# Optimization experiments

Hardware: AMD Instinct MI355X
Metric: run time of the kernel (lower is better)

## Reference

```python
import jax, jax.numpy as jnp
import numpy as np

B, N, DIM, H, DH = 2, 2048, 1024, 16, 64
SOFTCAP = 50.0
SCALE = DH ** -0.5
EPS = 1e-12


def _rmsnorm(x, gamma):
    # F.normalize (l2norm over last dim) * sqrt(dim) * (gamma + 1)
    norm = jnp.maximum(jnp.linalg.norm(x, axis=-1, keepdims=True), EPS)
    return (x / norm) * (DIM ** 0.5) * (gamma + 1.0)


def _rotate_half(t):
    # interleaved pairs: (x1, x2) -> (-x2, x1), as in rotary_embedding_torch
    t = t.reshape(*t.shape[:-1], -1, 2)
    x1, x2 = t[..., 0], t[..., 1]
    return jnp.stack((-x2, x1), axis=-1).reshape(*t.shape[:-2], -1)


def _apply_rotary(freqs, t):
    # freqs: [n, d] broadcast over [b, h, n, d]
    return t * jnp.cos(freqs) + _rotate_half(t) * jnp.sin(freqs)


def setup_inputs() -> dict:
    key = jax.random.key(0)
    k0, k1, k2, k3, k4 = jax.random.split(key, 5)
    x = jax.random.normal(k0, (B, N, DIM), jnp.float32)
    gamma = jax.random.normal(k1, (DIM,), jnp.float32) * 0.02
    w_qkv = jax.random.normal(k2, (DIM, 3 * H * DH), jnp.float32) * 0.02
    w_out = jax.random.normal(k3, (H * DH, DIM), jnp.float32) * 0.02
    rotary_emb = jax.random.normal(k4, (N, DH), jnp.float32)
    attn_mask = jnp.broadcast_to(jnp.tril(jnp.ones((N, N), bool)), (B, N, N))
    return {"x": x, "attn_mask": attn_mask, "rotary_emb": rotary_emb,
            "gamma": gamma, "w_qkv": w_qkv, "w_out": w_out}


def reference(x, attn_mask, rotary_emb, gamma, w_qkv, w_out):
    x = _rmsnorm(x, gamma)
    qkv = (x @ w_qkv).reshape(B, N, 3, H, DH)        # b n (qkv h d)
    qkv = jnp.transpose(qkv, (2, 0, 3, 1, 4))        # qkv b h n d
    q, k, v = qkv[0], qkv[1], qkv[2]
    q = _apply_rotary(rotary_emb, q)
    k = _apply_rotary(rotary_emb, k)
    q = q * SCALE
    sim = jnp.einsum('bhid,bhjd->bhij', q, k)
    sim = jnp.tanh(sim / SOFTCAP) * SOFTCAP          # softclamp
    mask_value = -jnp.finfo(sim.dtype).max
    sim = jnp.where(attn_mask[:, None, :, :], sim, mask_value)
    attn = jax.nn.softmax(sim, axis=-1)
    out = jnp.einsum('bhij,bhjd->bhid', attn, v)
    out = jnp.transpose(out, (0, 2, 1, 3)).reshape(B, N, H * DH)  # b n (h d)
    return out @ w_out
```

## Files before the change

### kernel.cpp

```cpp
#include <hip/hip_runtime.h>
#include <hip/hip_bf16.h>

typedef unsigned short u16;
typedef unsigned int u32;
typedef __bf16 bf16x8 __attribute__((ext_vector_type(8)));
typedef float f32x4 __attribute__((ext_vector_type(4)));

#define NB 2
#define NSEQ 2048
#define NDIM 1024
#define NH 16
#define NDH 64

static __device__ __forceinline__ u16 f2bf(float f) {
  return __builtin_bit_cast(u16, (__bf16)f);
}
static __device__ __forceinline__ float bf2f(u16 u) {
  union { u32 u; float f; } a; a.u = ((u32)u) << 16; return a.f;
}
static __device__ __forceinline__ bf16x8 ldbf8(const u16* p) {
  return *(const bf16x8*)p;
}
static __device__ __forceinline__ f32x4 mfma16(bf16x8 a, bf16x8 b, f32x4 c) {
  return __builtin_amdgcn_mfma_f32_16x16x32_bf16(a, b, c, 0, 0, 0);
}
static __device__ __forceinline__ float fexp2(float x) {
  return __builtin_amdgcn_exp2f(x);
}
#define GLDS(g, d) __builtin_amdgcn_global_load_lds(                         \
    (const __attribute__((address_space(1))) void*)(g),                      \
    (__attribute__((address_space(3))) void*)(d), 16, 0, 0)

__global__ __launch_bounds__(256) void k_transpose(const float* __restrict__ in,
                                                   u16* __restrict__ out,
                                                   int R, int C) {
  __shared__ u16 tile[64][65];
  const int r0 = blockIdx.x * 64, c0 = blockIdx.y * 64;
  const int t = threadIdx.x;
  const int tr = t >> 6;
  const int tc = t & 63;
#pragma unroll 4
  for (int p = 0; p < 16; p++) {
    int r = p * 4 + tr;
    tile[r][tc] = f2bf(in[(size_t)(r0 + r) * C + (c0 + tc)]);
  }
  __syncthreads();
#pragma unroll 4
  for (int p = 0; p < 16; p++) {
    int rr = p * 4 + tr;
    out[(size_t)(c0 + rr) * R + (r0 + tc)] = tile[tc][rr];
  }
}

__global__ __launch_bounds__(256) void k_rmsnorm(const float* __restrict__ x,
                                                 const float* __restrict__ gamma,
                                                 u16* __restrict__ xn) {
  __shared__ float part[4];
  const int row = blockIdx.x;
  const int t = threadIdx.x;
  const float4 v = ((const float4*)(x + (size_t)row * NDIM))[t];
  float ss = v.x * v.x + v.y * v.y + v.z * v.z + v.w * v.w;
#pragma unroll
  for (int off = 1; off < 64; off <<= 1) ss += __shfl_xor(ss, off, 64);
  if ((t & 63) == 0) part[t >> 6] = ss;
  __syncthreads();
  const float tot = part[0] + part[1] + part[2] + part[3];
  const float scale = 32.0f / fmaxf(sqrtf(tot), 1e-12f);
  const float4 g = ((const float4*)gamma)[t];
  u16 o0 = f2bf(v.x * scale * (g.x + 1.0f));
  u16 o1 = f2bf(v.y * scale * (g.y + 1.0f));
  u16 o2 = f2bf(v.z * scale * (g.z + 1.0f));
  u16 o3 = f2bf(v.w * scale * (g.w + 1.0f));
  uint2 pv;
  pv.x = (u32)o0 | ((u32)o1 << 16);
  pv.y = (u32)o2 | ((u32)o3 << 16);
  *(uint2*)(xn + (size_t)row * NDIM + t * 4) = pv;
}

template <int EPI>
__global__ __launch_bounds__(256) void k_gemm_bt(const u16* __restrict__ A,
                                                 const u16* __restrict__ BT,
                                                 float* __restrict__ Of,
                                                 u16* __restrict__ O0,
                                                 u16* __restrict__ O1,
                                                 u16* __restrict__ O2) {
  constexpr int KD = 1024, BK = 64, NT = KD / BK;
  __shared__ u16 As[128 * BK];
  __shared__ u16 Bs[128 * BK];
  const int m0 = blockIdx.x * 128, n0 = blockIdx.y * 128;
  const int t = threadIdx.x;
  const int w = t >> 6, l = t & 63, lo = l & 15, hi = l >> 4;
  const int wr = (w >> 1) * 64, wc = (w & 1) * 64;
  const int srow = w * 32 + (l >> 3);
  const int sch  = (l & 7) ^ (l >> 3);
  const u16* ag = A  + (size_t)(m0 + srow) * KD + sch * 8;
  const u16* bg = BT + (size_t)(n0 + srow) * KD + sch * 8;
  u16* asd = As + w * 2048;
  u16* bsd = Bs + w * 2048;
  f32x4 acc[4][4] = {};
  for (int kt = 0; kt < NT; kt++) {
    const int k0 = kt * BK;
    __syncthreads();
#pragma unroll
    for (int i = 0; i < 4; i++) {
      GLDS(ag + k0 + i * 8 * KD, asd + i * 512);
      GLDS(bg + k0 + i * 8 * KD, bsd + i * 512);
    }
    __syncthreads();
    bf16x8 af[4][2], bb[4][2];
#pragma unroll
    for (int i = 0; i < 4; i++) {
      const int Ra = wr + i * 16 + lo, xa = Ra & 7;
      af[i][0] = ldbf8(&As[Ra * 64 + ((hi ^ xa) << 3)]);
      af[i][1] = ldbf8(&As[Ra * 64 + (((4 + hi) ^ xa) << 3)]);
      const int Rb = wc + i * 16 + lo, xb = Rb & 7;
      bb[i][0] = ldbf8(&Bs[Rb * 64 + ((hi ^ xb) << 3)]);
      bb[i][1] = ldbf8(&Bs[Rb * 64 + (((4 + hi) ^ xb) << 3)]);
    }
#pragma unroll
    for (int i = 0; i < 4; i++)
#pragma unroll
      for (int j = 0; j < 4; j++) {
        acc[i][j] = mfma16(af[i][0], bb[j][0], acc[i][j]);
        acc[i][j] = mfma16(af[i][1], bb[j][1], acc[i][j]);
      }
  }
#pragma unroll
  for (int i = 0; i < 4; i++) {
#pragma unroll
    for (int j = 0; j < 4; j++) {
      const int gr0 = m0 + wr + i * 16 + hi * 4;
      const int gc = n0 + wc + j * 16 + lo;
#pragma unroll
      for (int r = 0; r < 4; r++) {
        const int row = gr0 + r;
        if (EPI == 0) {
          Of[(size_t)row * 1024 + gc] = acc[i][j][r];
        } else {
          const u16 bv = f2bf(acc[i][j][r]);
          const int which = gc >> 10, rem = gc & 1023;
          const int h = rem >> 6, dh = rem & 63;
          const int b = row >> 11, ns = row & 2047;
          if (which == 2) {
            O2[(((size_t)b * NH + h) * NDH + dh) * NSEQ + ns] = bv;
          } else {
            const size_t idx = ((((size_t)b * NH + h) * NSEQ) + ns) * NDH + dh;
            (which == 0 ? O0 : O1)[idx] = bv;
          }
        }
      }
    }
  }
}

__global__ __launch_bounds__(256) void k_rotprep(const float* __restrict__ rot,
                                                 float4* __restrict__ tab) {
  const int i = blockIdx.x * 256 + threadIdx.x;
  const int n = i >> 5, p = i & 31;
  const float fe = rot[n * NDH + 2 * p], fo = rot[n * NDH + 2 * p + 1];
  float ce, se, co, so;
  __sincosf(fe, &se, &ce);
  __sincosf(fo, &so, &co);
  tab[i] = make_float4(ce, se, co, so);
}

__global__ __launch_bounds__(256) void k_rotary(u16* __restrict__ qb,
                                                u16* __restrict__ kb,
                                                const float4* __restrict__ tab) {
  const int gi = blockIdx.x * 256 + threadIdx.x;
  const int half = gi >> 19;
  const int i = gi & ((1 << 19) - 1);
  u16* buf = half ? kb : qb;
  const float scale = half ? 1.0f : 0.125f;
  const int p0 = (i & 7) * 4;
  const int n = (i >> 3) & (NSEQ - 1);
  union { uint4 v; u16 s[8]; } u;
  u.v = *(const uint4*)(buf + (size_t)i * 8);
  union { uint4 v; u16 s[8]; } o;
#pragma unroll
  for (int pp = 0; pp < 4; pp++) {
    const float4 tb = tab[n * 32 + p0 + pp];
    const float a = bf2f(u.s[2 * pp]), b = bf2f(u.s[2 * pp + 1]);
    o.s[2 * pp]     = f2bf((a * tb.x - b * tb.y) * scale);
    o.s[2 * pp + 1] = f2bf((b * tb.z + a * tb.w) * scale);
  }
  *(uint4*)(buf + (size_t)i * 8) = o.v;
}

#define KCH(row, ch) ((((ch) ^ ((row) & 7)) * 8))
__global__ __launch_bounds__(128) void k_attn(const u16* __restrict__ Q,
                                              const u16* __restrict__ K,
                                              const u16* __restrict__ Vt,
                                              u16* __restrict__ O) {
  __shared__ u16 Ks[2][2048];
  __shared__ u16 Vs[2][2048];
  __shared__ u16 Ps[2][16][40];
  const int qt = 63 - (blockIdx.x >> 5);
  const int bh = blockIdx.x & 31;
  const int b = bh >> 4, h = bh & 15;
  const size_t base = (size_t)bh * (NSEQ * NDH);
  const int t = threadIdx.x;
  const int w = t >> 6, l = t & 63, lq = l & 15, hf = l >> 4;
  const int rl = l >> 3;
  const int sc8 = ((l & 7) ^ rl) * 8;
  const int vr = l >> 2;
  const int q0 = qt * 32;
  const int nkt = qt + 1;
  const int rowg = q0 + w * 16 + hf * 4;

  bf16x8 aq0, aq1;
  {
    const u16* qp = Q + base + (size_t)(q0 + w * 16 + lq) * NDH;
    aq0 = ldbf8(qp + hf * 8);
    aq1 = ldbf8(qp + 32 + hf * 8);
  }
  f32x4 accO[4] = {};
  float lp[4] = {0.f, 0.f, 0.f, 0.f};

#define STAGE(bb, kt_)                                                        \
  {                                                                           \
    _Pragma("unroll")                                                         \
    for (int i_ = 0; i_ < 2; i_++) {                                          \
      const int ii = w * 2 + i_;                                              \
      GLDS(K + base + (size_t)((kt_) * 32 + ii * 8 + rl) * NDH + sc8,         \
           &Ks[bb][ii * 512]);                                                \
      const int dR = ii * 16 + vr;                                            \
      const int vc = (((l & 3) ^ (dR & 3) ^ ((dR >> 2) & 3))) * 8;            \
      GLDS(Vt + base + (size_t)dR * NSEQ + (kt_) * 32 + vc,                   \
           &Vs[bb][ii * 512]);                                                \
    }                                                                         \
  }

  int cur = 0;
  STAGE(0, 0);

  for (int kt = 0; kt < nkt; kt++) {
    __syncthreads();
    if (kt + 1 < nkt) STAGE(cur ^ 1, kt + 1);
    const u16* ks = Ks[cur];
    const u16* vs = Vs[cur];

    f32x4 s[2];
#pragma unroll
    for (int nt = 0; nt < 2; nt++) {
      const int kr = nt * 16 + lq;
      f32x4 z = {};
      z = mfma16(aq0, ldbf8(&ks[kr * 64 + KCH(kr, hf)]), z);
      z = mfma16(aq1, ldbf8(&ks[kr * 64 + KCH(kr, 4 + hf)]), z);
      s[nt] = z;
    }
    const bool diag = (kt == qt);
#pragma unroll
    for (int nt = 0; nt < 2; nt++) {
      const int col = kt * 32 + nt * 16 + lq;
#pragma unroll
      for (int r = 0; r < 4; r++) {
        const float v = s[nt][r];
        const float uu = v * v;
        const float poly = fmaf(uu, fmaf(uu, 2.1333333e-8f, -1.3333333e-4f), 1.0f);
        float p = fexp2(v * 1.44269504f * poly);
        if (diag && col > rowg + r) p = 0.0f;
        s[nt][r] = p;
        lp[r] += p;
      }
    }
#pragma unroll
    for (int nt = 0; nt < 2; nt++)
#pragma unroll
      for (int r = 0; r < 4; r++)
        Ps[w][hf * 4 + r][nt * 16 + lq] = f2bf(s[nt][r]);

    const bf16x8 ap0 = ldbf8(&Ps[w][lq][hf * 8]);
    const int vph = (hf ^ (lq & 3) ^ ((lq >> 2) & 3)) * 8;
#pragma unroll
    for (int dt = 0; dt < 4; dt++) {
      const int d = dt * 16 + lq;
      accO[dt] = mfma16(ap0, ldbf8(&vs[d * 32 + vph]), accO[dt]);
    }
    cur ^= 1;
  }
  float lr[4];
#pragma unroll
  for (int r = 0; r < 4; r++) {
    float lv = lp[r];
    lv += __shfl_xor(lv, 1, 64);
    lv += __shfl_xor(lv, 2, 64);
    lv += __shfl_xor(lv, 4, 64);
    lv += __shfl_xor(lv, 8, 64);
    lr[r] = __builtin_amdgcn_rcpf(lv);
  }
#pragma unroll
  for (int dt = 0; dt < 4; dt++) {
#pragma unroll
    for (int r = 0; r < 4; r++) {
      const int row = rowg + r;
      const float v = accO[dt][r] * lr[r];
      const size_t idx = (((size_t)(b * NSEQ + row)) * NH + h) * NDH + dt * 16 + lq;
      O[idx] = f2bf(v);
    }
  }
#undef STAGE
}

extern "C" void kernel_launch(void* const* d_in, const int* in_sizes, int n_in,
                              void* d_out, int out_size, void* d_ws, size_t ws_size,
                              hipStream_t stream) {
  const float* x     = (const float*)d_in[0];
  const float* rot   = (const float*)d_in[2];
  const float* gamma = (const float*)d_in[3];
  const float* wqkv  = (const float*)d_in[4];
  const float* wout  = (const float*)d_in[5];

  char* ws = (char*)d_ws;
  u16* xn    = (u16*)(ws);
  u16* wqkvT = (u16*)(ws + (size_t)( 8u << 20));
  u16* woutT = (u16*)(ws + (size_t)(14u << 20));
  u16* qb    = (u16*)(ws + (size_t)(16u << 20));
  u16* kb    = (u16*)(ws + (size_t)(24u << 20));
  u16* vt    = (u16*)(ws + (size_t)(32u << 20));
  float4* rtab = (float4*)(ws);
  u16* ob    = xn;

  k_transpose<<<dim3(16, 48), 256, 0, stream>>>(wqkv, wqkvT, 1024, 3072);
  k_transpose<<<dim3(16, 16), 256, 0, stream>>>(wout, woutT, 1024, 1024);
  k_rmsnorm<<<4096, 256, 0, stream>>>(x, gamma, xn);
  k_gemm_bt<1><<<dim3(32, 24), 256, 0, stream>>>(xn, wqkvT, nullptr, qb, kb, vt);
  k_rotprep<<<256, 256, 0, stream>>>(rot, rtab);
  k_rotary<<<4096, 256, 0, stream>>>(qb, kb, rtab);
  k_attn<<<2048, 128, 0, stream>>>(qb, kb, vt, ob);
  k_gemm_bt<0><<<dim3(32, 8), 256, 0, stream>>>(ob, woutT, (float*)d_out, nullptr, nullptr, nullptr);
}
```

Before: 143.4 us.

## Pair causal query tiles per block, widen KV tiles, fuse Q rotary into attention

```diff
diff --git a/kernel.cpp b/kernel.cpp
--- a/kernel.cpp
+++ b/kernel.cpp
@@ -164,139 +164,175 @@
   tab[i] = make_float4(ce, se, co, so);
 }
 
-__global__ __launch_bounds__(256) void k_rotary(u16* __restrict__ qb,
-                                                u16* __restrict__ kb,
+__global__ __launch_bounds__(256) void k_rotary(u16* __restrict__ kb,
                                                 const float4* __restrict__ tab) {
-  const int gi = blockIdx.x * 256 + threadIdx.x;
-  const int half = gi >> 19;
-  const int i = gi & ((1 << 19) - 1);
-  u16* buf = half ? kb : qb;
-  const float scale = half ? 1.0f : 0.125f;
+  const int i = blockIdx.x * 256 + threadIdx.x;
   const int p0 = (i & 7) * 4;
   const int n = (i >> 3) & (NSEQ - 1);
   union { uint4 v; u16 s[8]; } u;
-  u.v = *(const uint4*)(buf + (size_t)i * 8);
+  u.v = *(const uint4*)(kb + (size_t)i * 8);
   union { uint4 v; u16 s[8]; } o;
 #pragma unroll
   for (int pp = 0; pp < 4; pp++) {
     const float4 tb = tab[n * 32 + p0 + pp];
     const float a = bf2f(u.s[2 * pp]), b = bf2f(u.s[2 * pp + 1]);
-    o.s[2 * pp]     = f2bf((a * tb.x - b * tb.y) * scale);
-    o.s[2 * pp + 1] = f2bf((b * tb.z + a * tb.w) * scale);
-  }
-  *(uint4*)(buf + (size_t)i * 8) = o.v;
+    o.s[2 * pp]     = f2bf(a * tb.x - b * tb.y);
+    o.s[2 * pp + 1] = f2bf(b * tb.z + a * tb.w);
+  }
+  *(uint4*)(kb + (size_t)i * 8) = o.v;
 }
 
 #define KCH(row, ch) ((((ch) ^ ((row) & 7)) * 8))
 __global__ __launch_bounds__(128) void k_attn(const u16* __restrict__ Q,
                                               const u16* __restrict__ K,
                                               const u16* __restrict__ Vt,
+                                              const float4* __restrict__ rtab,
                                               u16* __restrict__ O) {
-  __shared__ u16 Ks[2][2048];
-  __shared__ u16 Vs[2][2048];
-  __shared__ u16 Ps[2][16][40];
-  const int qt = 63 - (blockIdx.x >> 5);
+  __shared__ u16 Ks[2][4096];
+  __shared__ u16 Vs[2][4096];
+  __shared__ u16 Ps[2][16][64];
+  const int pr = blockIdx.x >> 5;
   const int bh = blockIdx.x & 31;
   const int b = bh >> 4, h = bh & 15;
   const size_t base = (size_t)bh * (NSEQ * NDH);
   const int t = threadIdx.x;
   const int w = t >> 6, l = t & 63, lq = l & 15, hf = l >> 4;
+
   const int rl = l >> 3;
   const int sc8 = ((l & 7) ^ rl) * 8;
-  const int vr = l >> 2;
-  const int q0 = qt * 32;
-  const int nkt = qt + 1;
-  const int rowg = q0 + w * 16 + hf * 4;
-
-  bf16x8 aq0, aq1;
-  {
-    const u16* qp = Q + base + (size_t)(q0 + w * 16 + lq) * NDH;
-    aq0 = ldbf8(qp + hf * 8);
-    aq1 = ldbf8(qp + 32 + hf * 8);
-  }
-  f32x4 accO[4] = {};
-  float lp[4] = {0.f, 0.f, 0.f, 0.f};
+
+  const u16* kR[4];
+  const u16* vR[4];
+#pragma unroll
+  for (int i_ = 0; i_ < 4; i_++) {
+    const int R_ = (w * 4 + i_) * 8 + rl;
+    kR[i_] = K + base + (size_t)R_ * NDH + sc8;
+    vR[i_] = Vt + base + (size_t)R_ * NSEQ + sc8;
+  }
 
 #define STAGE(bb, kt_)                                                        \
   {                                                                           \
     _Pragma("unroll")                                                         \
-    for (int i_ = 0; i_ < 2; i_++) {                                          \
-      const int ii = w * 2 + i_;                                              \
-      GLDS(K + base + (size_t)((kt_) * 32 + ii * 8 + rl) * NDH + sc8,         \
-           &Ks[bb][ii * 512]);                                                \
-      const int dR = ii * 16 + vr;                                            \
-      const int vc = (((l & 3) ^ (dR & 3) ^ ((dR >> 2) & 3))) * 8;            \
-      GLDS(Vt + base + (size_t)dR * NSEQ + (kt_) * 32 + vc,                   \
-           &Vs[bb][ii * 512]);                                                \
+    for (int i_ = 0; i_ < 4; i_++) {                                          \
+      GLDS(kR[i_] + (size_t)(kt_) * (64 * NDH), &Ks[bb][(w * 4 + i_) * 512]); \
+      GLDS(vR[i_] + (kt_) * 64, &Vs[bb][(w * 4 + i_) * 512]);                 \
     }                                                                         \
   }
 
   int cur = 0;
-  STAGE(0, 0);
-
-  for (int kt = 0; kt < nkt; kt++) {
+  STAGE(0, pr * 0);
+
+#pragma unroll
+  for (int half = 0; half < 2; half++) {
+    const int qt = half ? (63 - pr) : pr;
+    const int q0 = qt * 32;
+    const int nkt = (qt >> 1) + 1;
+    const int ktd = nkt - 1;
+    const int rowg = q0 + w * 16 + hf * 4;
+
+    bf16x8 aq0, aq1;
+    {
+      const u16* qp = Q + base + (size_t)(q0 + w * 16 + lq) * NDH;
+      union { bf16x8 v; u16 s[8]; } r0, r1, o0, o1;
+      r0.v = ldbf8(qp + hf * 8);
+      r1.v = ldbf8(qp + 32 + hf * 8);
+      const float4* rt = rtab + (size_t)(q0 + w * 16 + lq) * 32;
+#pragma unroll
+      for (int m = 0; m < 4; m++) {
+        const float4 t0 = rt[hf * 4 + m];
+        const float a0 = bf2f(r0.s[2 * m]), b0 = bf2f(r0.s[2 * m + 1]);
+        o0.s[2 * m]     = f2bf((a0 * t0.x - b0 * t0.y) * 0.125f);
+        o0.s[2 * m + 1] = f2bf((b0 * t0.z + a0 * t0.w) * 0.125f);
+        const float4 t1 = rt[16 + hf * 4 + m];
+        const float a1 = bf2f(r1.s[2 * m]), b1 = bf2f(r1.s[2 * m + 1]);
+        o1.s[2 * m]     = f2bf((a1 * t1.x - b1 * t1.y) * 0.125f);
+        o1.s[2 * m + 1] = f2bf((b1 * t1.z + a1 * t1.w) * 0.125f);
+      }
+      aq0 = o0.v;
+      aq1 = o1.v;
+    }
+    f32x4 accO[4] = {};
+    float lp[4] = {0.f, 0.f, 0.f, 0.f};
+
+#define QTILE(KT, DIAG)                                                       \
+    {                                                                         \
+      const u16* ks = Ks[cur];                                                \
+      const u16* vs = Vs[cur];                                                \
+      f32x4 s[4];                                                             \
+      _Pragma("unroll")                                                       \
+      for (int nt = 0; nt < 4; nt++) {                                        \
+        const int kr = nt * 16 + lq;                                          \
+        f32x4 z = {};                                                         \
+        z = mfma16(aq0, ldbf8(&ks[kr * 64 + KCH(kr, hf)]), z);                \
+        z = mfma16(aq1, ldbf8(&ks[kr * 64 + KCH(kr, 4 + hf)]), z);            \
+        s[nt] = z;                                                            \
+      }                                                                       \
+      _Pragma("unroll")                                                       \
+      for (int nt = 0; nt < 4; nt++) {                                        \
+        _Pragma("unroll")                                                     \
+        for (int r = 0; r < 4; r++) {                                         \
+          const float v = s[nt][r];                                           \
+          const float uu = v * v;                                             \
+          float p = fexp2(v * fmaf(uu, fmaf(uu, 3.0777855e-8f,                \
+                                            -1.9235932e-4f), 1.44269504f));  \
+          if (DIAG) {                                                         \
+            const int col = (KT) * 64 + nt * 16 + lq;                         \
+            if (col > rowg + r) p = 0.0f;                                     \
+          }                                                                   \
+          s[nt][r] = p;                                                       \
+          lp[r] += p;                                                         \
+        }                                                                     \
+      }                                                                       \
+      _Pragma("unroll")                                                       \
+      for (int nt = 0; nt < 4; nt++)                                          \
+        _Pragma("unroll")                                                     \
+        for (int r = 0; r < 4; r++) {                                         \
+          const int row = hf * 4 + r;                                         \
+          Ps[w][row][KCH(row, 2 * nt + (lq >> 3)) + (lq & 7)] =               \
+              f2bf(s[nt][r]);                                                 \
+        }                                                                     \
+      const bf16x8 ap0 = ldbf8(&Ps[w][lq][KCH(lq, hf)]);                      \
+      const bf16x8 ap1 = ldbf8(&Ps[w][lq][KCH(lq, 4 + hf)]);                  \
+      _Pragma("unroll")                                                       \
+      for (int dt = 0; dt < 4; dt++) {                                        \
+        const int d = dt * 16 + lq;                                           \
+        accO[dt] = mfma16(ap0, ldbf8(&vs[d * 64 + KCH(d, hf)]), accO[dt]);    \
+        accO[dt] = mfma16(ap1, ldbf8(&vs[d * 64 + KCH(d, 4 + hf)]), accO[dt]);\
+      }                                                                       \
+    }
+
+    for (int kt = 0; kt < ktd; kt++) {
+      __syncthreads();
+      STAGE(cur ^ 1, kt + 1);
+      QTILE(kt, false);
+      cur ^= 1;
+    }
     __syncthreads();
-    if (kt + 1 < nkt) STAGE(cur ^ 1, kt + 1);
-    const u16* ks = Ks[cur];
-    const u16* vs = Vs[cur];
-
-    f32x4 s[2];
-#pragma unroll
-    for (int nt = 0; nt < 2; nt++) {
-      const int kr = nt * 16 + lq;
-      f32x4 z = {};
-      z = mfma16(aq0, ldbf8(&ks[kr * 64 + KCH(kr, hf)]), z);
-      z = mfma16(aq1, ldbf8(&ks[kr * 64 + KCH(kr, 4 + hf)]), z);
-      s[nt] = z;
-    }
-    const bool diag = (kt == qt);
-#pragma unroll
-    for (int nt = 0; nt < 2; nt++) {
-      const int col = kt * 32 + nt * 16 + lq;
+    if (half == 0) STAGE(cur ^ 1, 0);
+    QTILE(ktd, true);
+    cur ^= 1;
+#undef QTILE
+
+    float lr[4];
+#pragma unroll
+    for (int r = 0; r < 4; r++) {
+      float lv = lp[r];
+      lv += __shfl_xor(lv, 1, 64);
+      lv += __shfl_xor(lv, 2, 64);
+      lv += __shfl_xor(lv, 4, 64);
+      lv += __shfl_xor(lv, 8, 64);
+      lr[r] = __builtin_amdgcn_rcpf(lv);
+    }
+#pragma unroll
+    for (int dt = 0; dt < 4; dt++) {
 #pragma unroll
       for (int r = 0; r < 4; r++) {
-        const float v = s[nt][r];
-        const float uu = v * v;
-        const float poly = fmaf(uu, fmaf(uu, 2.1333333e-8f, -1.3333333e-4f), 1.0f);
-        float p = fexp2(v * 1.44269504f * poly);
-        if (diag && col > rowg + r) p = 0.0f;
-        s[nt][r] = p;
-        lp[r] += p;
+        const int row = rowg + r;
+        const float v = accO[dt][r] * lr[r];
+        const size_t idx =
+            (((size_t)(b * NSEQ + row)) * NH + h) * NDH + dt * 16 + lq;
+        O[idx] = f2bf(v);
       }
-    }
-#pragma unroll
-    for (int nt = 0; nt < 2; nt++)
-#pragma unroll
-      for (int r = 0; r < 4; r++)
-        Ps[w][hf * 4 + r][nt * 16 + lq] = f2bf(s[nt][r]);
-
-    const bf16x8 ap0 = ldbf8(&Ps[w][lq][hf * 8]);
-    const int vph = (hf ^ (lq & 3) ^ ((lq >> 2) & 3)) * 8;
-#pragma unroll
-    for (int dt = 0; dt < 4; dt++) {
-      const int d = dt * 16 + lq;
-      accO[dt] = mfma16(ap0, ldbf8(&vs[d * 32 + vph]), accO[dt]);
-    }
-    cur ^= 1;
-  }
-  float lr[4];
-#pragma unroll
-  for (int r = 0; r < 4; r++) {
-    float lv = lp[r];
-    lv += __shfl_xor(lv, 1, 64);
-    lv += __shfl_xor(lv, 2, 64);
-    lv += __shfl_xor(lv, 4, 64);
-    lv += __shfl_xor(lv, 8, 64);
-    lr[r] = __builtin_amdgcn_rcpf(lv);
-  }
-#pragma unroll
-  for (int dt = 0; dt < 4; dt++) {
-#pragma unroll
-    for (int r = 0; r < 4; r++) {
-      const int row = rowg + r;
-      const float v = accO[dt][r] * lr[r];
-      const size_t idx = (((size_t)(b * NSEQ + row)) * NH + h) * NDH + dt * 16 + lq;
-      O[idx] = f2bf(v);
     }
   }
 #undef STAGE
@@ -318,7 +354,7 @@
   u16* qb    = (u16*)(ws + (size_t)(16u << 20));
   u16* kb    = (u16*)(ws + (size_t)(24u << 20));
   u16* vt    = (u16*)(ws + (size_t)(32u << 20));
-  float4* rtab = (float4*)(ws);
+  float4* rtab = (float4*)(ws + (size_t)(8u << 20));
   u16* ob    = xn;
 
   k_transpose<<<dim3(16, 48), 256, 0, stream>>>(wqkv, wqkvT, 1024, 3072);
@@ -326,7 +362,7 @@
   k_rmsnorm<<<4096, 256, 0, stream>>>(x, gamma, xn);
   k_gemm_bt<1><<<dim3(32, 24), 256, 0, stream>>>(xn, wqkvT, nullptr, qb, kb, vt);
   k_rotprep<<<256, 256, 0, stream>>>(rot, rtab);
-  k_rotary<<<4096, 256, 0, stream>>>(qb, kb, rtab);
-  k_attn<<<2048, 128, 0, stream>>>(qb, kb, vt, ob);
+  k_rotary<<<2048, 256, 0, stream>>>(kb, rtab);
+  k_attn<<<1024, 128, 0, stream>>>(qb, kb, vt, rtab, ob);
   k_gemm_bt<0><<<dim3(32, 8), 256, 0, stream>>>(ob, woutT, (float*)d_out, nullptr, nullptr, nullptr);
 }
```

New measurement: 138.6 us. 1.03x faster.
